# Kernel optimization log

Measured on AMD Instinct MI355X. Metric: run time of the kernel, lower is better.

Reference implementation:

```python
import jax, jax.numpy as jnp
import numpy as np

IN_F = 4096      # in_features (d_model)
OUT_F = 16384    # out_features (4*d_model FFN)
N_TOK = 8192     # tokens = batch*seq
K = OUT_F // 2   # number of kept output rows (static for jit)


def setup_inputs() -> dict:
    key = jax.random.key(0)
    k1, k2, k3, k4 = jax.random.split(key, 4)
    data = jax.random.normal(k1, (N_TOK, IN_F), jnp.float32)
    weight = jax.random.normal(k2, (OUT_F, IN_F), jnp.float32) * 0.02
    bias = jax.random.normal(k3, (OUT_F,), jnp.float32) * 0.02
    # mask with exactly K ones at random positions (static count -> jit-safe)
    perm = jax.random.permutation(k4, OUT_F)
    mask = jnp.zeros((OUT_F,), jnp.int32).at[perm[:K]].set(1)
    return {"data": data, "weight": weight, "bias": bias, "mask": mask}


def reference(data, weight, bias, mask):
    # mask.nonzero()[0] -> selected output-feature indices (ascending, as torch)
    idx = jnp.nonzero(mask, size=K)[0]                 # [K]
    w_sel = jnp.take(weight, idx, axis=0)              # [K, IN_F] row gather
    b_sel = jnp.take(bias, idx, axis=0)                # [K]
    # F.linear: data @ w_sel^T + b_sel  -> [N_TOK, K]
    return jnp.einsum('ti,ki->tk', data, w_sel) + b_sel
```

## Files before the change

kernel.cpp:

```cpp
#include <hip/hip_runtime.h>
#include <hip/hip_bf16.h>

typedef __bf16 bf16_t;
typedef __attribute__((ext_vector_type(8))) __bf16 bf16x8;
typedef __attribute__((ext_vector_type(4))) float f32x4;

constexpr int IN_F  = 4096;
constexpr int OUT_F = 16384;
constexpr int N_TOK = 8192;
constexpr int KSEL  = 8192;
constexpr long A_ELEMS = (long)N_TOK * IN_F;

constexpr int BM = 256, BN = 256, BK = 64;
constexpr int NT = IN_F / BK;
constexpr int HALF_E = 128 * BK;

#define GLOBAL_CAST(p) (const __attribute__((address_space(1))) void*)(p)
#define LDS_CAST(p)    (__attribute__((address_space(3))) void*)(p)

__global__ __launch_bounds__(1024) void build_idx_kernel(
    const int* __restrict__ mask, const float* __restrict__ bias,
    int* __restrict__ idx, float* __restrict__ bsel)
{
    const int t    = threadIdx.x;
    const int lane = t & 63;
    const int wave = t >> 6;
    const int base_i = t * 16;

    int m[16];
    const int4* mp = (const int4*)(mask + base_i);
#pragma unroll
    for (int v = 0; v < 4; ++v) {
        int4 q = mp[v];
        m[v*4+0] = q.x; m[v*4+1] = q.y; m[v*4+2] = q.z; m[v*4+3] = q.w;
    }
    int cnt = 0;
#pragma unroll
    for (int j = 0; j < 16; ++j) cnt += (m[j] != 0) ? 1 : 0;

    int incl = cnt;
#pragma unroll
    for (int d = 1; d < 64; d <<= 1) {
        int o = __shfl_up(incl, (unsigned)d);
        if (lane >= d) incl += o;
    }

    __shared__ int wsum[16];
    __shared__ int wbase[16];
    if (lane == 63) wsum[wave] = incl;
    __syncthreads();
    if (t == 0) {
        int s = 0;
        for (int w = 0; w < 16; ++w) { wbase[w] = s; s += wsum[w]; }
    }
    __syncthreads();

    int p = wbase[wave] + (incl - cnt);
#pragma unroll
    for (int j = 0; j < 16; ++j) {
        if (m[j]) {
            int i = base_i + j;
            idx[p]  = i;
            bsel[p] = bias[i];
            ++p;
        }
    }
}

__global__ __launch_bounds__(256) void convert_kernel(
    const float* __restrict__ A, const float* __restrict__ W,
    const int* __restrict__ idx,
    bf16_t* __restrict__ Ab, bf16_t* __restrict__ Wb)
{
    const long nvecA = A_ELEMS / 8;
    const long total = nvecA * 2;
    const long stride = (long)gridDim.x * blockDim.x;
    for (long v = (long)blockIdx.x * blockDim.x + threadIdx.x; v < total; v += stride) {
        const float4* src;
        bf16_t* dst;
        if (v < nvecA) {
            src = (const float4*)(A + v * 8);
            dst = Ab + v * 8;
        } else {
            long u = v - nvecA;
            int j = (int)(u >> 9);
            int k = (int)(u & 511) * 8;
            src = (const float4*)(W + (long)idx[j] * IN_F + k);
            dst = Wb + u * 8;
        }
        float4 x = src[0], y = src[1];
        bf16x8 o;
        o[0]=(bf16_t)x.x; o[1]=(bf16_t)x.y; o[2]=(bf16_t)x.z; o[3]=(bf16_t)x.w;
        o[4]=(bf16_t)y.x; o[5]=(bf16_t)y.y; o[6]=(bf16_t)y.z; o[7]=(bf16_t)y.w;
        *(bf16x8*)dst = o;
    }
}

__global__ __launch_bounds__(512, 2) void gemm8p_kernel(
    const bf16_t* __restrict__ A, const bf16_t* __restrict__ B,
    const float* __restrict__ bsel, float* __restrict__ C)
{
    __shared__ __attribute__((aligned(16))) bf16_t As[2][2][HALF_E];
    __shared__ __attribute__((aligned(16))) bf16_t Bs[2][2][HALF_E];

    const int tid  = threadIdx.x;
    const int w    = tid >> 6;
    const int lane = tid & 63;
    const int wr   = w >> 2;
    const int wc   = w & 3;

    const int bid = blockIdx.x;
    const int swz = (bid & 7) * 128 + (bid >> 3);
    const int m0 = (swz & 31) * BM;
    const int n0 = (swz >> 5) * BN;

    const int pr  = lane >> 3;
    const int csw = ((lane & 7) ^ pr) * 8;
    const bf16_t* aSrc[2][2];
    const bf16_t* bSrc[2][2];
#pragma unroll
    for (int h = 0; h < 2; ++h)
#pragma unroll
        for (int j = 0; j < 2; ++j) {
            const int row = h * 128 + (w * 2 + j) * 8 + pr;
            aSrc[h][j] = A + (long)(m0 + row) * IN_F + csw;
            bSrc[h][j] = B + (long)(n0 + row) * IN_F + csw;
        }

#define STAGE_AT(buf, tl) do {                                                 \
    _Pragma("unroll") for (int h = 0; h < 2; ++h)                              \
    _Pragma("unroll") for (int j = 0; j < 2; ++j)                              \
        __builtin_amdgcn_global_load_lds(                                      \
            GLOBAL_CAST(aSrc[h][j] + (long)(tl) * BK),                         \
            LDS_CAST(&As[buf][h][(w * 2 + j) * 512]), 16, 0, 0);               \
} while (0)
#define STAGE_BT(buf, tl) do {                                                 \
    _Pragma("unroll") for (int h = 0; h < 2; ++h)                              \
    _Pragma("unroll") for (int j = 0; j < 2; ++j)                              \
        __builtin_amdgcn_global_load_lds(                                      \
            GLOBAL_CAST(bSrc[h][j] + (long)(tl) * BK),                         \
            LDS_CAST(&Bs[buf][h][(w * 2 + j) * 512]), 16, 0, 0);               \
} while (0)

    f32x4 acc[8][4];
#pragma unroll
    for (int m = 0; m < 8; ++m)
#pragma unroll
        for (int n = 0; n < 4; ++n)
#pragma unroll
            for (int j = 0; j < 4; ++j) acc[m][n][j] = 0.f;

    const int fr    = lane & 15;
    const int kslot = lane >> 4;
    const int sp0 = ((kslot     ^ (fr & 7)) << 3);
    const int sp1 = (((4+kslot) ^ (fr & 7)) << 3);

    bf16x8 af[4][2], bg[4][2];

#define RDA(buf, mq) do {                                                      \
    _Pragma("unroll") for (int mm = 0; mm < 4; ++mm) {                         \
        const int r = ((mq) * 4 + mm) * 16 + fr;                               \
        af[mm][0] = *(const bf16x8*)&As[buf][wr][r * 64 + sp0];                \
        af[mm][1] = *(const bf16x8*)&As[buf][wr][r * 64 + sp1];                \
    } } while (0)
#define RDB_ALL(buf) do {                                                      \
    _Pragma("unroll") for (int nn = 0; nn < 4; ++nn) {                         \
        const int r = (wc & 1) * 64 + nn * 16 + fr;                            \
        bg[nn][0] = *(const bf16x8*)&Bs[buf][wc >> 1][r * 64 + sp0];           \
        bg[nn][1] = *(const bf16x8*)&Bs[buf][wc >> 1][r * 64 + sp1];           \
    } } while (0)
#define MFMAQ2(mq) do {                                                        \
    __builtin_amdgcn_s_setprio(1);                                             \
    _Pragma("unroll") for (int mm = 0; mm < 4; ++mm)                           \
    _Pragma("unroll") for (int nn = 0; nn < 4; ++nn) {                         \
        const int m = (mq) * 4 + mm;                                           \
        acc[m][nn] = __builtin_amdgcn_mfma_f32_16x16x32_bf16(                  \
            af[mm][0], bg[nn][0], acc[m][nn], 0, 0, 0);                        \
        acc[m][nn] = __builtin_amdgcn_mfma_f32_16x16x32_bf16(                  \
            af[mm][1], bg[nn][1], acc[m][nn], 0, 0, 0);                        \
    }                                                                          \
    __builtin_amdgcn_s_setprio(0); } while (0)
#define BAR()    __builtin_amdgcn_s_barrier()
#define LGKM0()  asm volatile("s_waitcnt lgkmcnt(0)" ::: "memory")
#define VMC4()   asm volatile("s_waitcnt vmcnt(4)" ::: "memory")
#define VMC0()   asm volatile("s_waitcnt vmcnt(0)" ::: "memory")

    STAGE_BT(0, 0); STAGE_AT(0, 0); STAGE_BT(1, 1);
    VMC4(); BAR();

    for (int I = 0; I < NT / 2; ++I) {
        const int t = 2 * I, u = t + 1;
        const bool s2 = (I < NT / 2 - 1);

        RDA(0, 0); RDB_ALL(0);
        STAGE_AT(1, u);
        BAR(); LGKM0(); MFMAQ2(0); BAR();

        RDA(0, 1);
        if (s2) STAGE_BT(0, t + 2);
        BAR(); LGKM0(); MFMAQ2(1);
        if (s2) VMC4(); else VMC0();
        BAR();

        RDA(1, 0); RDB_ALL(1);
        if (s2) STAGE_AT(0, t + 2);
        BAR(); LGKM0(); MFMAQ2(0); BAR();

        RDA(1, 1);
        if (s2) STAGE_BT(1, u + 2);
        BAR(); LGKM0(); MFMAQ2(1);
        if (s2) VMC4();
        BAR();
    }
    VMC0();

#undef STAGE_AT
#undef STAGE_BT
#undef RDA
#undef RDB_ALL
#undef MFMAQ2
#undef BAR
#undef LGKM0
#undef VMC4
#undef VMC0

    float b4[4];
#pragma unroll
    for (int n = 0; n < 4; ++n) b4[n] = bsel[n0 + wc * 64 + n * 16 + fr];

    const int rbase = m0 + wr * 128 + kslot * 4;
#pragma unroll
    for (int m = 0; m < 8; ++m)
#pragma unroll
        for (int n = 0; n < 4; ++n) {
            const int col = n0 + wc * 64 + n * 16 + fr;
#pragma unroll
            for (int j = 0; j < 4; ++j)
                C[(long)(rbase + m * 16 + j) * KSEL + col] = acc[m][n][j] + b4[n];
        }
}

__global__ __launch_bounds__(256) void gemm_f32staged_kernel(
    const float* __restrict__ A, const float* __restrict__ W,
    const int* __restrict__ idx, const float* __restrict__ bsel,
    float* __restrict__ C)
{
    constexpr int FBM = 128, FBN = 128, BK2 = 32;
    __shared__ __attribute__((aligned(16))) float Asf[FBM * BK2];
    __shared__ __attribute__((aligned(16))) float Bsf[FBN * BK2];

    const int tid  = threadIdx.x;
    const int wave = tid >> 6;
    const int lane = tid & 63;
    const int wrf  = wave >> 1;
    const int wcf  = wave & 1;

    const int m0 = blockIdx.x * FBM;
    const int n0 = blockIdx.y * FBN;

    const int srow = lane >> 3;
    const int scol = (lane & 7) * 4;

    const float* aptr[4];
    const float* bptr[4];
#pragma unroll
    for (int i = 0; i < 4; ++i) {
        aptr[i] = A + (long)(m0 + wave * 32 + i * 8 + srow) * IN_F + scol;
        const int br = idx[n0 + wave * 32 + i * 8 + srow];
        bptr[i] = W + (long)br * IN_F + scol;
    }

    f32x4 acc[4][4];
#pragma unroll
    for (int m = 0; m < 4; ++m)
#pragma unroll
        for (int n = 0; n < 4; ++n)
#pragma unroll
            for (int j = 0; j < 4; ++j) acc[m][n][j] = 0.f;

    const int fr = lane & 15;
    const int fk = (lane >> 4) * 8;

    for (int k0 = 0; k0 < IN_F; k0 += BK2) {
#pragma unroll
        for (int i = 0; i < 4; ++i) {
            __builtin_amdgcn_global_load_lds(GLOBAL_CAST(aptr[i] + k0),
                LDS_CAST(&Asf[(wave * 32 + i * 8) * BK2]), 16, 0, 0);
            __builtin_amdgcn_global_load_lds(GLOBAL_CAST(bptr[i] + k0),
                LDS_CAST(&Bsf[(wave * 32 + i * 8) * BK2]), 16, 0, 0);
        }
        __syncthreads();

        bf16x8 af[4], bg[4];
#pragma unroll
        for (int m = 0; m < 4; ++m) {
            const float* p = &Asf[(wrf * 64 + m * 16 + fr) * BK2 + fk];
            f32x4 x = *(const f32x4*)p, y = *(const f32x4*)(p + 4);
#pragma unroll
            for (int j = 0; j < 4; ++j) { af[m][j] = (bf16_t)x[j]; af[m][4+j] = (bf16_t)y[j]; }
        }
#pragma unroll
        for (int n = 0; n < 4; ++n) {
            const float* p = &Bsf[(wcf * 64 + n * 16 + fr) * BK2 + fk];
            f32x4 x = *(const f32x4*)p, y = *(const f32x4*)(p + 4);
#pragma unroll
            for (int j = 0; j < 4; ++j) { bg[n][j] = (bf16_t)x[j]; bg[n][4+j] = (bf16_t)y[j]; }
        }
#pragma unroll
        for (int m = 0; m < 4; ++m)
#pragma unroll
            for (int n = 0; n < 4; ++n)
                acc[m][n] = __builtin_amdgcn_mfma_f32_16x16x32_bf16(
                    af[m], bg[n], acc[m][n], 0, 0, 0);
        __syncthreads();
    }

    float b4[4];
#pragma unroll
    for (int n = 0; n < 4; ++n) b4[n] = bsel[n0 + wcf * 64 + n * 16 + fr];

    const int rbase = m0 + wrf * 64 + (lane >> 4) * 4;
#pragma unroll
    for (int m = 0; m < 4; ++m)
#pragma unroll
        for (int n = 0; n < 4; ++n) {
            const int col = n0 + wcf * 64 + n * 16 + fr;
#pragma unroll
            for (int j = 0; j < 4; ++j)
                C[(long)(rbase + m * 16 + j) * KSEL + col] = acc[m][n][j] + b4[n];
        }
}

extern "C" void kernel_launch(void* const* d_in, const int* in_sizes, int n_in,
                              void* d_out, int out_size, void* d_ws, size_t ws_size,
                              hipStream_t stream)
{
    const float* data   = (const float*)d_in[0];
    const float* weight = (const float*)d_in[1];
    const float* bias   = (const float*)d_in[2];
    const int*   mask   = (const int*)d_in[3];
    float*       out    = (float*)d_out;

    char* ws = (char*)d_ws;
    int*   idx  = (int*)ws;
    float* bsel = (float*)(ws + (KSEL * 4));
    bf16_t* Ab  = (bf16_t*)(ws + (KSEL * 8));
    bf16_t* Wb  = Ab + A_ELEMS;

    const size_t NEED = (size_t)KSEL * 8 + (size_t)A_ELEMS * 2 * 2;

    build_idx_kernel<<<1, 1024, 0, stream>>>(mask, bias, idx, bsel);

    if (ws_size >= NEED) {
        convert_kernel<<<2048, 256, 0, stream>>>(data, weight, idx, Ab, Wb);
        gemm8p_kernel<<<1024, 512, 0, stream>>>(Ab, Wb, bsel, out);
    } else {
        dim3 grid(N_TOK / 128, KSEL / 128);
        gemm_f32staged_kernel<<<grid, 256, 0, stream>>>(data, weight, idx, bsel, out);
    }
}
```

Baseline: 723.9 us.

## Switch GEMM to 32x32x16 MFMA tiles with flat LDS layout

```diff
diff --git a/kernel.cpp b/kernel.cpp
--- a/kernel.cpp
+++ b/kernel.cpp
@@ -4,6 +4,7 @@
 typedef __bf16 bf16_t;
 typedef __attribute__((ext_vector_type(8))) __bf16 bf16x8;
 typedef __attribute__((ext_vector_type(4))) float f32x4;
+typedef __attribute__((ext_vector_type(16))) float f32x16;
 
 constexpr int IN_F  = 4096;
 constexpr int OUT_F = 16384;
@@ -13,7 +14,7 @@
 
 constexpr int BM = 256, BN = 256, BK = 64;
 constexpr int NT = IN_F / BK;
-constexpr int HALF_E = 128 * BK;
+constexpr int TILE_E = BM * BK;
 
 #define GLOBAL_CAST(p) (const __attribute__((address_space(1))) void*)(p)
 #define LDS_CAST(p)    (__attribute__((address_space(3))) void*)(p)
@@ -96,12 +97,12 @@
     }
 }
 
-__global__ __launch_bounds__(512, 2) void gemm8p_kernel(
+__global__ __launch_bounds__(512, 2) void gemm32_kernel(
     const bf16_t* __restrict__ A, const bf16_t* __restrict__ B,
     const float* __restrict__ bsel, float* __restrict__ C)
 {
-    __shared__ __attribute__((aligned(16))) bf16_t As[2][2][HALF_E];
-    __shared__ __attribute__((aligned(16))) bf16_t Bs[2][2][HALF_E];
+    __shared__ __attribute__((aligned(16))) bf16_t As[2][TILE_E];
+    __shared__ __attribute__((aligned(16))) bf16_t Bs[2][TILE_E];
 
     const int tid  = threadIdx.x;
     const int w    = tid >> 6;
@@ -116,69 +117,63 @@
 
     const int pr  = lane >> 3;
     const int csw = ((lane & 7) ^ pr) * 8;
-    const bf16_t* aSrc[2][2];
-    const bf16_t* bSrc[2][2];
-#pragma unroll
-    for (int h = 0; h < 2; ++h)
-#pragma unroll
-        for (int j = 0; j < 2; ++j) {
-            const int row = h * 128 + (w * 2 + j) * 8 + pr;
-            aSrc[h][j] = A + (long)(m0 + row) * IN_F + csw;
-            bSrc[h][j] = B + (long)(n0 + row) * IN_F + csw;
-        }
+    const bf16_t* aSrc[4];
+    const bf16_t* bSrc[4];
+#pragma unroll
+    for (int j = 0; j < 4; ++j) {
+        const int row = w * 32 + j * 8 + pr;
+        aSrc[j] = A + (long)(m0 + row) * IN_F + csw;
+        bSrc[j] = B + (long)(n0 + row) * IN_F + csw;
+    }
 
 #define STAGE_AT(buf, tl) do {                                                 \
-    _Pragma("unroll") for (int h = 0; h < 2; ++h)                              \
-    _Pragma("unroll") for (int j = 0; j < 2; ++j)                              \
+    _Pragma("unroll") for (int j = 0; j < 4; ++j)                              \
         __builtin_amdgcn_global_load_lds(                                      \
-            GLOBAL_CAST(aSrc[h][j] + (long)(tl) * BK),                         \
-            LDS_CAST(&As[buf][h][(w * 2 + j) * 512]), 16, 0, 0);               \
+            GLOBAL_CAST(aSrc[j] + (long)(tl) * BK),                            \
+            LDS_CAST(&As[buf][(w * 32 + j * 8) * BK]), 16, 0, 0);              \
 } while (0)
 #define STAGE_BT(buf, tl) do {                                                 \
-    _Pragma("unroll") for (int h = 0; h < 2; ++h)                              \
-    _Pragma("unroll") for (int j = 0; j < 2; ++j)                              \
+    _Pragma("unroll") for (int j = 0; j < 4; ++j)                              \
         __builtin_amdgcn_global_load_lds(                                      \
-            GLOBAL_CAST(bSrc[h][j] + (long)(tl) * BK),                         \
-            LDS_CAST(&Bs[buf][h][(w * 2 + j) * 512]), 16, 0, 0);               \
+            GLOBAL_CAST(bSrc[j] + (long)(tl) * BK),                            \
+            LDS_CAST(&Bs[buf][(w * 32 + j * 8) * BK]), 16, 0, 0);              \
 } while (0)
 
-    f32x4 acc[8][4];
-#pragma unroll
-    for (int m = 0; m < 8; ++m)
-#pragma unroll
-        for (int n = 0; n < 4; ++n)
-#pragma unroll
-            for (int j = 0; j < 4; ++j) acc[m][n][j] = 0.f;
-
-    const int fr    = lane & 15;
-    const int kslot = lane >> 4;
-    const int sp0 = ((kslot     ^ (fr & 7)) << 3);
-    const int sp1 = (((4+kslot) ^ (fr & 7)) << 3);
-
-    bf16x8 af[4][2], bg[4][2];
-
-#define RDA(buf, mq) do {                                                      \
-    _Pragma("unroll") for (int mm = 0; mm < 4; ++mm) {                         \
-        const int r = ((mq) * 4 + mm) * 16 + fr;                               \
-        af[mm][0] = *(const bf16x8*)&As[buf][wr][r * 64 + sp0];                \
-        af[mm][1] = *(const bf16x8*)&As[buf][wr][r * 64 + sp1];                \
+    f32x16 acc[4][2];
+#pragma unroll
+    for (int m = 0; m < 4; ++m)
+#pragma unroll
+        for (int n = 0; n < 2; ++n)
+#pragma unroll
+            for (int j = 0; j < 16; ++j) acc[m][n][j] = 0.f;
+
+    const int rA = lane & 31;
+    const int lh = lane >> 5;
+    int spk[4];
+#pragma unroll
+    for (int ks = 0; ks < 4; ++ks) spk[ks] = (((2 * ks + lh) ^ (rA & 7)) << 3);
+
+    bf16x8 af[2][4], bg[2][4];
+
+#define RDA(buf, half) do {                                                    \
+    _Pragma("unroll") for (int mm = 0; mm < 2; ++mm) {                         \
+        const int r = wr * 128 + ((half) * 2 + mm) * 32 + rA;                  \
+        _Pragma("unroll") for (int ks = 0; ks < 4; ++ks)                       \
+            af[mm][ks] = *(const bf16x8*)&As[buf][r * 64 + spk[ks]];           \
     } } while (0)
 #define RDB_ALL(buf) do {                                                      \
-    _Pragma("unroll") for (int nn = 0; nn < 4; ++nn) {                         \
-        const int r = (wc & 1) * 64 + nn * 16 + fr;                            \
-        bg[nn][0] = *(const bf16x8*)&Bs[buf][wc >> 1][r * 64 + sp0];           \
-        bg[nn][1] = *(const bf16x8*)&Bs[buf][wc >> 1][r * 64 + sp1];           \
+    _Pragma("unroll") for (int nn = 0; nn < 2; ++nn) {                         \
+        const int r = wc * 64 + nn * 32 + rA;                                  \
+        _Pragma("unroll") for (int ks = 0; ks < 4; ++ks)                       \
+            bg[nn][ks] = *(const bf16x8*)&Bs[buf][r * 64 + spk[ks]];           \
     } } while (0)
-#define MFMAQ2(mq) do {                                                        \
+#define MFMAQ(half) do {                                                       \
     __builtin_amdgcn_s_setprio(1);                                             \
-    _Pragma("unroll") for (int mm = 0; mm < 4; ++mm)                           \
-    _Pragma("unroll") for (int nn = 0; nn < 4; ++nn) {                         \
-        const int m = (mq) * 4 + mm;                                           \
-        acc[m][nn] = __builtin_amdgcn_mfma_f32_16x16x32_bf16(                  \
-            af[mm][0], bg[nn][0], acc[m][nn], 0, 0, 0);                        \
-        acc[m][nn] = __builtin_amdgcn_mfma_f32_16x16x32_bf16(                  \
-            af[mm][1], bg[nn][1], acc[m][nn], 0, 0, 0);                        \
-    }                                                                          \
+    _Pragma("unroll") for (int mm = 0; mm < 2; ++mm)                           \
+    _Pragma("unroll") for (int nn = 0; nn < 2; ++nn)                           \
+    _Pragma("unroll") for (int ks = 0; ks < 4; ++ks)                           \
+        acc[(half)*2+mm][nn] = __builtin_amdgcn_mfma_f32_32x32x16_bf16(        \
+            af[mm][ks], bg[nn][ks], acc[(half)*2+mm][nn], 0, 0, 0);            \
     __builtin_amdgcn_s_setprio(0); } while (0)
 #define BAR()    __builtin_amdgcn_s_barrier()
 #define LGKM0()  asm volatile("s_waitcnt lgkmcnt(0)" ::: "memory")
@@ -194,21 +189,21 @@
 
         RDA(0, 0); RDB_ALL(0);
         STAGE_AT(1, u);
-        BAR(); LGKM0(); MFMAQ2(0); BAR();
+        BAR(); LGKM0(); MFMAQ(0); BAR();
 
         RDA(0, 1);
         if (s2) STAGE_BT(0, t + 2);
-        BAR(); LGKM0(); MFMAQ2(1);
+        BAR(); LGKM0(); MFMAQ(1);
         if (s2) VMC4(); else VMC0();
         BAR();
 
         RDA(1, 0); RDB_ALL(1);
         if (s2) STAGE_AT(0, t + 2);
-        BAR(); LGKM0(); MFMAQ2(0); BAR();
+        BAR(); LGKM0(); MFMAQ(0); BAR();
 
         RDA(1, 1);
         if (s2) STAGE_BT(1, u + 2);
-        BAR(); LGKM0(); MFMAQ2(1);
+        BAR(); LGKM0(); MFMAQ(1);
         if (s2) VMC4();
         BAR();
     }
@@ -218,26 +213,29 @@
 #undef STAGE_BT
 #undef RDA
 #undef RDB_ALL
-#undef MFMAQ2
+#undef MFMAQ
 #undef BAR
 #undef LGKM0
 #undef VMC4
 #undef VMC0
 
-    float b4[4];
-#pragma unroll
-    for (int n = 0; n < 4; ++n) b4[n] = bsel[n0 + wc * 64 + n * 16 + fr];
-
-    const int rbase = m0 + wr * 128 + kslot * 4;
-#pragma unroll
-    for (int m = 0; m < 8; ++m)
-#pragma unroll
-        for (int n = 0; n < 4; ++n) {
-            const int col = n0 + wc * 64 + n * 16 + fr;
-#pragma unroll
-            for (int j = 0; j < 4; ++j)
-                C[(long)(rbase + m * 16 + j) * KSEL + col] = acc[m][n][j] + b4[n];
-        }
+    float b2[2];
+#pragma unroll
+    for (int n = 0; n < 2; ++n) b2[n] = bsel[n0 + wc * 64 + n * 32 + rA];
+
+#pragma unroll
+    for (int mt = 0; mt < 4; ++mt) {
+        const int rbase = m0 + wr * 128 + mt * 32 + 4 * lh;
+#pragma unroll
+        for (int nt = 0; nt < 2; ++nt) {
+            const int col = n0 + wc * 64 + nt * 32 + rA;
+#pragma unroll
+            for (int reg = 0; reg < 16; ++reg) {
+                const int row = rbase + (reg & 3) + 8 * (reg >> 2);
+                C[(long)row * KSEL + col] = acc[mt][nt][reg] + b2[nt];
+            }
+        }
+    }
 }
 
 __global__ __launch_bounds__(256) void gemm_f32staged_kernel(
@@ -353,7 +351,7 @@
 
     if (ws_size >= NEED) {
         convert_kernel<<<2048, 256, 0, stream>>>(data, weight, idx, Ab, Wb);
-        gemm8p_kernel<<<1024, 512, 0, stream>>>(Ab, Wb, bsel, out);
+        gemm32_kernel<<<1024, 512, 0, stream>>>(Ab, Wb, bsel, out);
     } else {
         dim3 grid(N_TOK / 128, KSEL / 128);
         gemm_f32staged_kernel<<<grid, 256, 0, stream>>>(data, weight, idx, bsel, out);
```

Measured after the change: 846.2 us. 16.9% more time.
